# Kernel optimization log

Measured on AMD Instinct MI355X. Metric: run time of the kernel, lower is better.

The kernel has to match this reference:

```python
import jax, jax.numpy as jnp
import numpy as np

N_NODES = 100000
N_EDGES = 3200000
N_GRAPHS = 512
IN_DIM = 128
H1, H2 = 32, 64
OUT_DIM = 1
LN_EPS = 1e-5


def setup_inputs() -> dict:
    key = jax.random.key(0)
    ks = jax.random.split(key, 12)
    x = jax.random.normal(ks[0], (N_NODES, IN_DIM), dtype=jnp.float32)
    edge_index = jax.random.randint(ks[1], (2, N_EDGES), 0, N_NODES, dtype=jnp.int64)
    batch = jnp.sort(jax.random.randint(ks[2], (N_NODES,), 0, N_GRAPHS, dtype=jnp.int64))
    def lin(k, fi, fo):
        s = 1.0 / np.sqrt(fi)
        return jax.random.uniform(k, (fi, fo), minval=-s, maxval=s, dtype=jnp.float32)
    params = {
        'W1': lin(ks[3], IN_DIM, H1), 'b1': jnp.zeros((H1,), jnp.float32),
        'g1': jnp.ones((H1,), jnp.float32), 'be1': jnp.zeros((H1,), jnp.float32),
        'W2': lin(ks[4], H1, H2), 'b2': jnp.zeros((H2,), jnp.float32),
        'g2': jnp.ones((H2,), jnp.float32), 'be2': jnp.zeros((H2,), jnp.float32),
        'Wc1': lin(ks[5], H2, 32), 'bc1': jnp.zeros((32,), jnp.float32),
        'Wc2': lin(ks[6], 32, OUT_DIM), 'bc2': jnp.zeros((OUT_DIM,), jnp.float32),
    }
    return {'x': x, 'edge_index': edge_index, 'batch': batch, **params}


def _gcn_norm(edge_index, n):
    # add self loops (PyG GCNConv default)
    loop = jnp.arange(n, dtype=edge_index.dtype)
    src = jnp.concatenate([edge_index[0], loop])
    dst = jnp.concatenate([edge_index[1], loop])
    deg = jax.ops.segment_sum(jnp.ones_like(dst, dtype=jnp.float32), dst, num_segments=n)
    dinv = jnp.where(deg > 0, 1.0 / jnp.sqrt(deg), 0.0)
    norm = dinv[src] * dinv[dst]  # [E+N]
    return src, dst, norm


def _gcn_conv(x, src, dst, norm, W, b, n):
    h = x @ W                                    # tiny GEMM
    msg = h[src] * norm[:, None]                 # gather + scale (memory-bound)
    agg = jax.ops.segment_sum(msg, dst, num_segments=n)  # scatter-add
    return agg + b


def _layernorm(x, g, b):
    mu = jnp.mean(x, axis=-1, keepdims=True)
    var = jnp.mean(jnp.square(x - mu), axis=-1, keepdims=True)
    return (x - mu) * jax.lax.rsqrt(var + LN_EPS) * g + b


def reference(x, edge_index, batch, W1, b1, g1, be1, W2, b2, g2, be2, Wc1, bc1, Wc2, bc2):
    n = x.shape[0]
    src, dst, norm = _gcn_norm(edge_index, n)
    # layer 1: GCNConv -> LayerNorm -> ReLU (dropout = identity in eval)
    h = jax.nn.relu(_layernorm(_gcn_conv(x, src, dst, norm, W1, b1, n), g1, be1))
    # layer 2
    h = jax.nn.relu(_layernorm(_gcn_conv(h, src, dst, norm, W2, b2, n), g2, be2))
    # global mean pool over graphs
    sums = jax.ops.segment_sum(h, batch, num_segments=N_GRAPHS)
    cnts = jax.ops.segment_sum(jnp.ones((n,), h.dtype), batch, num_segments=N_GRAPHS)
    pooled = sums / jnp.maximum(cnts, 1.0)[:, None]  # [G, H2]
    # classifier MLP
    z = jax.nn.relu(pooled @ Wc1 + bc1)
    return z @ Wc2 + bc2
```

## Files before the change

kernel.cpp:

```cpp
#include <hip/hip_runtime.h>
#include <hip/hip_fp16.h>

#define CAP 10240

__global__ __launch_bounds__(1024) void k_fused1(const int* __restrict__ ei,
                                                 const float* __restrict__ x,
                                                 const float* __restrict__ W1,
                                                 const int* __restrict__ batch,
                                                 int* __restrict__ gcnt,
                                                 int* __restrict__ bucketed,
                                                 __half* __restrict__ hs,
                                                 int* __restrict__ gstart,
                                                 int nA, int nG1, int NB,
                                                 int n, int E, int G) {
    __shared__ __align__(16) char smem[40960];
    int tid = threadIdx.x;
    int bid = blockIdx.x;
    if (bid < nA) {
        int* hist = (int*)smem;
        int* excl = hist + 512;
        int* gb   = excl + 512;
        int* ebuf = gb + 512;
        const int* src = ei;
        const int* dst = ei + E;
        for (int i = tid; i < 512; i += 1024) hist[i] = 0;
        __syncthreads();
        int e0 = bid * 8192;
        int d[8], sR[8];
#pragma unroll
        for (int k = 0; k < 8; k++) {
            int e = e0 + k * 1024 + tid;
            bool v = e < E;
            d[k]  = v ? dst[e] : -1;
            sR[k] = v ? src[e] : 0;
            if (v) atomicAdd(&hist[d[k] >> 8], 1);
        }
        __syncthreads();
        if (tid < 512) excl[tid] = hist[tid];
        __syncthreads();
        for (int off = 1; off < 512; off <<= 1) {
            int v2 = 0;
            if (tid < 512) v2 = excl[tid] + ((tid >= off) ? excl[tid - off] : 0);
            __syncthreads();
            if (tid < 512) excl[tid] = v2;
            __syncthreads();
        }
        if (tid < 512) {
            int c = hist[tid];
            int ex = excl[tid] - c;
            excl[tid] = ex;
            gb[tid] = c ? atomicAdd(&gcnt[tid], c) : 0;
            hist[tid] = ex;
        }
        __syncthreads();
#pragma unroll
        for (int k = 0; k < 8; k++) {
            if (d[k] >= 0) {
                int b = d[k] >> 8;
                int p = atomicAdd(&hist[b], 1);
                ebuf[p] = (sR[k] << 8) | (d[k] & 255);
            }
        }
        __syncthreads();
        if (tid < 512) {
            int lds0 = excl[tid];
            int cnt  = hist[tid] - lds0;
            int gb0  = gb[tid];
            int* dstp = bucketed + (size_t)tid * CAP;
            for (int k = 0; k < cnt; k++) {
                int gp = gb0 + k;
                if (gp < CAP) dstp[gp] = ebuf[lds0 + k];
            }
        }
    } else if (bid < nA + nG1) {
        float* Ws = (float*)smem;
        const float4* W4 = (const float4*)W1;
        ((float4*)Ws)[tid] = W4[tid];
        __syncthreads();
        int gb2 = bid - nA;
        int row = gb2 * 128 + (tid >> 3);
        int g8 = tid & 7;
        if (row >= n) return;
        const float4* x4 = (const float4*)x;
        const float4* Ws4 = (const float4*)Ws;
        float a0 = 0.f, a1 = 0.f, a2 = 0.f, a3 = 0.f;
#pragma unroll 4
        for (int j = 0; j < 32; j++) {
            float4 xq = x4[(size_t)row * 32 + j];
#pragma unroll
            for (int t = 0; t < 4; t++) {
                float xv = (t == 0) ? xq.x : (t == 1) ? xq.y : (t == 2) ? xq.z : xq.w;
                float4 wv = Ws4[(4 * j + t) * 8 + g8];
                a0 += xv * wv.x; a1 += xv * wv.y; a2 += xv * wv.z; a3 += xv * wv.w;
            }
        }
        __half2 o[2] = { __floats2half2_rn(a0, a1), __floats2half2_rn(a2, a3) };
        *(float2*)(hs + (size_t)row * 32 + g8 * 4) = *(const float2*)o;
    } else {
        int i = (bid - nA - nG1) * 1024 + tid;
        if (i > n) return;
        if (i == 0) {
            for (int g = 0; g <= batch[0]; g++) gstart[g] = 0;
        } else if (i == n) {
            for (int g = batch[n - 1] + 1; g <= G; g++) gstart[g] = n;
        } else {
            int b = batch[i], p = batch[i - 1];
            for (int g = p + 1; g <= b; g++) gstart[g] = i;
        }
    }
}

__global__ __launch_bounds__(512) void k_bucketB(const int* __restrict__ bucketed,
                                                 const int* __restrict__ gcnt,
                                                 int* __restrict__ csr,
                                                 int* __restrict__ offs,
                                                 int* __restrict__ deg,
                                                 float* __restrict__ dinv,
                                                 __half* __restrict__ hs, int n) {
    __shared__ int hist[256], scan_a[256], scan_b[256];
    __shared__ float sdinv[256];
    int b = blockIdx.x;
    int tid = threadIdx.x;
    int cnt = min(gcnt[b], CAP);
    int base = b * CAP;
    const int* ent = bucketed + (size_t)b * CAP;
    if (tid < 256) hist[tid] = 0;
    __syncthreads();
    for (int i = tid; i < cnt; i += 512) atomicAdd(&hist[ent[i] & 255], 1);
    __syncthreads();
    int h = (tid < 256) ? hist[tid] : 0;
    if (tid < 256) scan_a[tid] = h;
    __syncthreads();
    int* cur = scan_a;
    int* nxt = scan_b;
    for (int off = 1; off < 256; off <<= 1) {
        if (tid < 256) nxt[tid] = cur[tid] + ((tid >= off) ? cur[tid - off] : 0);
        __syncthreads();
        int* tmp = cur; cur = nxt; nxt = tmp;
    }
    if (tid < 256) {
        int ex = cur[tid] - h;
        float dv = rsqrtf((float)(h + 1));
        sdinv[tid] = dv;
        int node = b * 256 + tid;
        if (node < n) {
            offs[node] = base + ex;
            deg[node] = h;
            dinv[node] = dv;
        }
        hist[tid] = ex;
    }
    __syncthreads();
    for (int i = tid; i < cnt; i += 512) {
        int v = ent[i];
        int p = atomicAdd(&hist[v & 255], 1);
        csr[base + p] = v >> 8;
    }
    float4* hsv = (float4*)hs;
#pragma unroll
    for (int p = 0; p < 2; p++) {
        int idx = p * 512 + tid;
        int nl = idx >> 2, cg = idx & 3;
        int node = b * 256 + nl;
        if (node < n) {
            float dv = sdinv[nl];
            float4 raw = hsv[(size_t)node * 4 + cg];
            __half2* h2 = (__half2*)&raw;
            __half2 o[4];
#pragma unroll
            for (int j = 0; j < 4; j++) {
                float2 f = __half22float2(h2[j]);
                o[j] = __floats2half2_rn(f.x * dv, f.y * dv);
            }
            hsv[(size_t)node * 4 + cg] = *(const float4*)o;
        }
    }
}

template <bool DO_LN>
__global__ __launch_bounds__(256) void k_gather(const __half* __restrict__ hs,
                                                const int* __restrict__ csr,
                                                const int* __restrict__ offs,
                                                const int* __restrict__ deg,
                                                const float* __restrict__ dinv,
                                                const float* __restrict__ b,
                                                const float* __restrict__ g,
                                                const float* __restrict__ be,
                                                __half* __restrict__ out, int n) {
    int wave = threadIdx.x >> 6;
    int lane = threadIdx.x & 63;
    int row = blockIdx.x * 4 + wave;
    if (row >= n) return;
    int nb = lane >> 2;
    int cg = lane & 3;
    int base = offs[row];
    int dg = deg[row];
    const float4* hsv = (const float4*)hs;
    float acc[8];
#pragma unroll
    for (int j = 0; j < 8; j++) acc[j] = 0.f;
    int nfull = dg & ~15;
    for (int it = 0; it < nfull; it += 16) {
        int s = csr[base + it + nb];
        float4 raw = hsv[(size_t)s * 4 + cg];
        const __half2* h2 = (const __half2*)&raw;
#pragma unroll
        for (int j = 0; j < 4; j++) {
            float2 f = __half22float2(h2[j]);
            acc[2 * j]     += f.x;
            acc[2 * j + 1] += f.y;
        }
    }
    if (nfull + nb < dg) {
        int s = csr[base + nfull + nb];
        float4 raw = hsv[(size_t)s * 4 + cg];
        const __half2* h2 = (const __half2*)&raw;
#pragma unroll
        for (int j = 0; j < 4; j++) {
            float2 f = __half22float2(h2[j]);
            acc[2 * j]     += f.x;
            acc[2 * j + 1] += f.y;
        }
    }
#pragma unroll
    for (int m = 4; m <= 32; m <<= 1)
#pragma unroll
        for (int j = 0; j < 8; j++) acc[j] += __shfl_xor(acc[j], m, 64);
    float dv = dinv[row];
    float4 sraw = hsv[(size_t)row * 4 + cg];
    const __half2* sh2 = (const __half2*)&sraw;
    float a[8];
#pragma unroll
    for (int j = 0; j < 4; j++) {
        float2 f = __half22float2(sh2[j]);
        a[2 * j]     = (acc[2 * j]     + f.x) * dv;
        a[2 * j + 1] = (acc[2 * j + 1] + f.y) * dv;
    }
    if (DO_LN) {
        int c0 = cg * 8;
        float s = 0.f;
#pragma unroll
        for (int j = 0; j < 8; j++) { a[j] += b[c0 + j]; s += a[j]; }
#pragma unroll
        for (int m = 1; m <= 2; m <<= 1) s += __shfl_xor(s, m, 64);
        float mu = s * (1.0f / 32.0f);
        float v2 = 0.f;
#pragma unroll
        for (int j = 0; j < 8; j++) { a[j] -= mu; v2 += a[j] * a[j]; }
#pragma unroll
        for (int m = 1; m <= 2; m <<= 1) v2 += __shfl_xor(v2, m, 64);
        float inv = rsqrtf(v2 * (1.0f / 32.0f) + 1e-5f);
#pragma unroll
        for (int j = 0; j < 8; j++)
            a[j] = fmaxf(a[j] * inv * g[c0 + j] + be[c0 + j], 0.f) * dv;
    }
    if (nb == 0) {
        __half2 o[4];
#pragma unroll
        for (int j = 0; j < 4; j++) o[j] = __floats2half2_rn(a[2 * j], a[2 * j + 1]);
        ((float4*)out)[(size_t)row * 4 + cg] = *(const float4*)o;
    }
}

__global__ __launch_bounds__(512) void k_pool_cls(const __half* __restrict__ agg2,
                                                  const float* __restrict__ W2,
                                                  const float* __restrict__ b2,
                                                  const float* __restrict__ g2,
                                                  const float* __restrict__ be2,
                                                  const int* __restrict__ gstart,
                                                  const float* __restrict__ Wc1,
                                                  const float* __restrict__ bc1,
                                                  const float* __restrict__ Wc2,
                                                  const float* __restrict__ bc2,
                                                  float* __restrict__ out) {
    __shared__ float Ws[32 * 64];
    __shared__ float red[8 * 64];
    int tid = threadIdx.x;
    for (int i = tid; i < 32 * 64; i += 512) Ws[i] = W2[i];
    int g = blockIdx.x;
    int r0 = gstart[g], r1 = gstart[g + 1];
    int wave = tid >> 6, lane = tid & 63;
    float pacc = 0.0f;
    __syncthreads();
    for (int row = r0 + wave; row < r1; row += 8) {
        const float4* a4 = (const float4*)(agg2 + (size_t)row * 32);
        float4 r4[4];
#pragma unroll
        for (int q = 0; q < 4; q++) r4[q] = a4[q];
        const __half2* ah = (const __half2*)r4;
        float acc = b2[lane];
#pragma unroll
        for (int k2 = 0; k2 < 16; k2++) {
            float2 f = __half22float2(ah[k2]);
            acc += f.x * Ws[(2 * k2) * 64 + lane] + f.y * Ws[(2 * k2 + 1) * 64 + lane];
        }
        float s = acc;
#pragma unroll
        for (int m = 32; m >= 1; m >>= 1) s += __shfl_xor(s, m, 64);
        float mu = s * (1.0f / 64.0f);
        float d = acc - mu;
        float v = d * d;
#pragma unroll
        for (int m = 32; m >= 1; m >>= 1) v += __shfl_xor(v, m, 64);
        float val = d * rsqrtf(v * (1.0f / 64.0f) + 1e-5f) * g2[lane] + be2[lane];
        pacc += fmaxf(val, 0.0f);
    }
    red[wave * 64 + lane] = pacc;
    __syncthreads();
    if (wave == 0) {
        float p = 0.f;
#pragma unroll
        for (int w = 0; w < 8; w++) p += red[w * 64 + lane];
        p *= 1.0f / fmaxf((float)(r1 - r0), 1.0f);
        red[lane] = p;
    }
    __syncthreads();
    if (wave == 0 && lane < 32) {
        float zs = bc1[lane];
#pragma unroll
        for (int k = 0; k < 64; k++) zs += red[k] * Wc1[k * 32 + lane];
        float o = fmaxf(zs, 0.0f) * Wc2[lane];
#pragma unroll
        for (int m = 16; m >= 1; m >>= 1) o += __shfl_xor(o, m, 64);
        if (lane == 0) out[g] = o + bc2[0];
    }
}


extern "C" void kernel_launch(void* const* d_in, const int* in_sizes, int n_in,
                              void* d_out, int out_size, void* d_ws, size_t ws_size,
                              hipStream_t stream) {
    const float* x     = (const float*)d_in[0];
    const int*   ei    = (const int*)d_in[1];
    const int*   batch = (const int*)d_in[2];
    const float* W1  = (const float*)d_in[3];
    const float* b1  = (const float*)d_in[4];
    const float* g1  = (const float*)d_in[5];
    const float* be1 = (const float*)d_in[6];
    const float* W2  = (const float*)d_in[7];
    const float* b2  = (const float*)d_in[8];
    const float* g2  = (const float*)d_in[9];
    const float* be2 = (const float*)d_in[10];
    const float* Wc1 = (const float*)d_in[11];
    const float* bc1 = (const float*)d_in[12];
    const float* Wc2 = (const float*)d_in[13];
    const float* bc2 = (const float*)d_in[14];

    int n = in_sizes[0] / 128;
    int E = in_sizes[1] / 2;
    int G = out_size;
    int NB = (n + 255) >> 8;

    float* ws     = (float*)d_ws;
    float* dinv   = ws;
    int*   deg    = (int*)(dinv + n);
    int*   offs   = deg + n;
    int*   gcnt   = offs + n;
    int*   gstart = gcnt + 512;
    int*   csr    = gstart + 516;
    __half* hsA   = (__half*)(csr + (size_t)NB * CAP);
    int*   bucketed = (int*)(hsA + (size_t)n * 32);
    __half* hsB   = (__half*)bucketed;

    int nA  = (E + 8191) / 8192;
    int nG1 = (n + 127) / 128;
    int nGs = (n + 1024) / 1024;

    hipMemsetAsync(gcnt, 0, 512 * sizeof(int), stream);

    k_fused1<<<nA + nG1 + nGs, 1024, 0, stream>>>(ei, x, W1, batch, gcnt, bucketed,
                                                  hsA, gstart, nA, nG1, NB, n, E, G);
    k_bucketB<<<NB, 512, 0, stream>>>(bucketed, gcnt, csr, offs, deg, dinv, hsA, n);

    k_gather<true><<<(n + 3) / 4, 256, 0, stream>>>(hsA, csr, offs, deg, dinv,
                                                    b1, g1, be1, hsB, n);
    k_gather<false><<<(n + 3) / 4, 256, 0, stream>>>(hsB, csr, offs, deg, dinv,
                                                     nullptr, nullptr, nullptr, hsA, n);
    k_pool_cls<<<G, 512, 0, stream>>>(hsA, W2, b2, g2, be2, gstart,
                                      Wc1, bc1, Wc2, bc2, (float*)d_out);
}
```

Measured before the change: 217.4 us.

## Pack four rows per wave in gather and prefetch neighbors with half accumulation

The neighbor-gather kernel now gives each node row 16 lanes instead of a full 64-lane wave, so one wave processes four rows. This cuts idle lanes for the typical degree of about 32. Each lane walks its neighbors with a two-deep software prefetch and two packed-half accumulators. The cross-lane reduction shrinks to two shuffle steps, and the launch grid is resized to match. Accumulating in fp16 before converting to fp32 adds rounding error that grows with node degree.

```diff
diff --git a/kernel.cpp b/kernel.cpp
--- a/kernel.cpp
+++ b/kernel.cpp
@@ -189,41 +189,46 @@
                                                 __half* __restrict__ out, int n) {
     int wave = threadIdx.x >> 6;
     int lane = threadIdx.x & 63;
-    int row = blockIdx.x * 4 + wave;
+    int q   = lane >> 4;
+    int l16 = lane & 15;
+    int nb  = l16 >> 2;
+    int cg  = l16 & 3;
+    int row = blockIdx.x * 16 + wave * 4 + q;
     if (row >= n) return;
-    int nb = lane >> 2;
-    int cg = lane & 3;
     int base = offs[row];
     int dg = deg[row];
     const float4* hsv = (const float4*)hs;
+    const float4 fz = make_float4(0.f, 0.f, 0.f, 0.f);
+    const __half2 hz = __floats2half2_rn(0.f, 0.f);
+    __half2 ha0[4], ha1[4];
+#pragma unroll
+    for (int j = 0; j < 4; j++) { ha0[j] = hz; ha1[j] = hz; }
+
+    int e = nb;
+    float4 r0 = (e     < dg) ? hsv[(size_t)csr[base + e    ] * 4 + cg] : fz;
+    float4 r1 = (e + 4 < dg) ? hsv[(size_t)csr[base + e + 4] * 4 + cg] : fz;
+    while (e < dg) {
+        float4 p0 = (e +  8 < dg) ? hsv[(size_t)csr[base + e +  8] * 4 + cg] : fz;
+        float4 p1 = (e + 12 < dg) ? hsv[(size_t)csr[base + e + 12] * 4 + cg] : fz;
+        const __half2* h0 = (const __half2*)&r0;
+        const __half2* h1 = (const __half2*)&r1;
+#pragma unroll
+        for (int j = 0; j < 4; j++) {
+            ha0[j] = __hadd2(ha0[j], h0[j]);
+            ha1[j] = __hadd2(ha1[j], h1[j]);
+        }
+        r0 = p0; r1 = p1; e += 8;
+    }
     float acc[8];
 #pragma unroll
-    for (int j = 0; j < 8; j++) acc[j] = 0.f;
-    int nfull = dg & ~15;
-    for (int it = 0; it < nfull; it += 16) {
-        int s = csr[base + it + nb];
-        float4 raw = hsv[(size_t)s * 4 + cg];
-        const __half2* h2 = (const __half2*)&raw;
-#pragma unroll
-        for (int j = 0; j < 4; j++) {
-            float2 f = __half22float2(h2[j]);
-            acc[2 * j]     += f.x;
-            acc[2 * j + 1] += f.y;
-        }
-    }
-    if (nfull + nb < dg) {
-        int s = csr[base + nfull + nb];
-        float4 raw = hsv[(size_t)s * 4 + cg];
-        const __half2* h2 = (const __half2*)&raw;
-#pragma unroll
-        for (int j = 0; j < 4; j++) {
-            float2 f = __half22float2(h2[j]);
-            acc[2 * j]     += f.x;
-            acc[2 * j + 1] += f.y;
-        }
-    }
-#pragma unroll
-    for (int m = 4; m <= 32; m <<= 1)
+    for (int j = 0; j < 4; j++) {
+        float2 f0 = __half22float2(ha0[j]);
+        float2 f1 = __half22float2(ha1[j]);
+        acc[2 * j]     = f0.x + f1.x;
+        acc[2 * j + 1] = f0.y + f1.y;
+    }
+#pragma unroll
+    for (int m = 4; m <= 8; m <<= 1)
 #pragma unroll
         for (int j = 0; j < 8; j++) acc[j] += __shfl_xor(acc[j], m, 64);
     float dv = dinv[row];
@@ -372,10 +377,10 @@
                                                   hsA, gstart, nA, nG1, NB, n, E, G);
     k_bucketB<<<NB, 512, 0, stream>>>(bucketed, gcnt, csr, offs, deg, dinv, hsA, n);
 
-    k_gather<true><<<(n + 3) / 4, 256, 0, stream>>>(hsA, csr, offs, deg, dinv,
-                                                    b1, g1, be1, hsB, n);
-    k_gather<false><<<(n + 3) / 4, 256, 0, stream>>>(hsB, csr, offs, deg, dinv,
-                                                     nullptr, nullptr, nullptr, hsA, n);
+    k_gather<true><<<(n + 15) / 16, 256, 0, stream>>>(hsA, csr, offs, deg, dinv,
+                                                      b1, g1, be1, hsB, n);
+    k_gather<false><<<(n + 15) / 16, 256, 0, stream>>>(hsB, csr, offs, deg, dinv,
+                                                       nullptr, nullptr, nullptr, hsA, n);
     k_pool_cls<<<G, 512, 0, stream>>>(hsA, W2, b2, g2, be2, gstart,
                                       Wc1, bc1, Wc2, bc2, (float*)d_out);
 }
```

After: 215.1 us. No clear change (-1.1%).
